# Optimization experiments

Hardware: AMD Instinct MI355X
Metric: run time of the kernel (lower is better)

The kernel has to match this reference:

```python
import jax, jax.numpy as jnp
import numpy as np

# physical constants / config (from __init__ defaults + chosen kwargs)
WFA_C = 4.6686e-13   # e/(4*pi*m_e*c) in 1/(G*Angstrom)
LAMBDA0 = 6301.5     # Angstrom
G_FACTOR = 1.5
WFA_WEIGHT = 0.5
STOKES_V = 3
BLOS_THRESH = 100.0
BASE_THRESH = 0.0004
TAU_IDX = np.array([0, 1, 2])
N_LOGTAU, N_MAGS = 21, 4
NWL = 112
START, END = 0, NWL - 1  # wavelength_range=None -> [0, len-1) slice
EPS = 1e-10


def _np_gradient(x):
    """np.gradient along last axis: central diffs interior, one-sided edges."""
    left = x[..., 1:2] - x[..., 0:1]
    mid = (x[..., 2:] - x[..., :-2]) * 0.5
    right = x[..., -1:] - x[..., -2:-1]
    return jnp.concatenate([left, mid, right], axis=-1)


def setup_inputs() -> dict:
    key = jax.random.key(0)
    kS, kP, kT = jax.random.split(key, 3)
    B = 65536
    input_stokes = jax.random.normal(kS, (B, 4, NWL), dtype=jnp.float32) * 0.01
    predicted_atm = jax.random.normal(kP, (B, N_LOGTAU * N_MAGS), dtype=jnp.float32)
    # target close to prediction so base MAE < base_loss_threshold -> WFA branch active
    target_atm = predicted_atm + 1e-4 * jax.random.normal(kT, (B, N_LOGTAU * N_MAGS), dtype=jnp.float32)
    wavelengths = jnp.linspace(6300.5, 6303.0, NWL).astype(jnp.float32)
    return {"input_stokes": input_stokes, "predicted_atm": predicted_atm,
            "target_atm": target_atm, "wavelengths": wavelengths}


def reference(input_stokes, predicted_atm, target_atm, wavelengths):
    # base MAE loss
    base_loss = jnp.mean(jnp.abs(predicted_atm - target_atm))

    # --- WFA B_LOS estimate, vectorized over batch ---
    wl = wavelengths[START:END]                      # [L]
    I = input_stokes[:, 0, START:END]                # [B, L]
    V = input_stokes[:, STOKES_V, START:END]         # [B, L]
    dI = _np_gradient(I) / _np_gradient(wl)[None, :]  # dI/dlambda, [B, L]

    # least squares V ~ p0*dI + p1; 2-column pinv == closed-form normal equations
    n = jnp.float32(dI.shape[-1])
    sd = jnp.sum(dI, axis=-1)
    sv = jnp.sum(V, axis=-1)
    sdd = jnp.sum(dI * dI, axis=-1)
    sdv = jnp.sum(dI * V, axis=-1)
    p0 = (n * sdv - sd * sv) / (n * sdd - sd * sd)   # slope, [B]
    wfa_blos = -p0 / (WFA_C * LAMBDA0 ** 2 * G_FACTOR)  # Gauss, [B]

    # predicted B_LOS: mean over tau_indices of last magnetic parameter
    atm = predicted_atm.reshape(-1, N_LOGTAU, N_MAGS)
    predicted_blos = atm[:, TAU_IDX, -1].mean(axis=1)  # [B]

    # thresholded masked log-abs MAE
    mask = jnp.abs(wfa_blos) < BLOS_THRESH
    diff = jnp.abs(jnp.log10(jnp.abs(predicted_blos) + EPS)
                   - jnp.log10(jnp.abs(wfa_blos) + EPS))
    cnt = jnp.sum(mask)
    wfa_loss_masked = jnp.sum(jnp.where(mask, diff, 0.0)) / jnp.maximum(cnt, 1).astype(diff.dtype)

    # early-return semantics: WFA only if base_loss < threshold AND any mask
    apply_wfa = (base_loss < BASE_THRESH) & (cnt > 0)
    wfa_loss = jnp.where(apply_wfa, wfa_loss_masked, jnp.float32(0.0))
    total_loss = jnp.where(apply_wfa,
                           (1.0 - WFA_WEIGHT) * base_loss + WFA_WEIGHT * wfa_loss_masked,
                           base_loss)
    return total_loss, base_loss, wfa_loss
```

## Files before the change

### kernel.cpp

```cpp
#include <hip/hip_runtime.h>
#include <math.h>

#define NWL   112
#define NCOLS 111
#define NATM  84
#define THREADS 256
#define WAVES_PER_BLOCK 4
#define MAIN_BLOCKS 2048

__device__ __forceinline__ float half_reduce_sum(float v) {
    v += __shfl_xor(v, 1,  64);
    v += __shfl_xor(v, 2,  64);
    v += __shfl_xor(v, 4,  64);
    v += __shfl_xor(v, 8,  64);
    v += __shfl_xor(v, 16, 64);
    return v;
}

__device__ __forceinline__ float wave_reduce_sum(float v) {
#pragma unroll
    for (int off = 32; off >= 1; off >>= 1)
        v += __shfl_xor(v, off, 64);
    return v;
}

__global__ __launch_bounds__(THREADS) void wfa_main(
    const float* __restrict__ stokes,
    const float* __restrict__ pred,
    const float* __restrict__ targ,
    const float* __restrict__ wl,
    float* __restrict__ ws,
    int nrows, int nblocks)
{
    __shared__ float s_idw[NWL];
    __shared__ float s_red[WAVES_PER_BLOCK][3];

    const int tid  = threadIdx.x;
    const int lane = tid & 63;
    const int wid  = tid >> 6;
    const int sub  = lane & 31;
    const int g    = lane & 32;

    if (tid < NWL) {
        const int j = tid;
        float d;
        if (j == 0)              d = wl[1] - wl[0];
        else if (j == NCOLS - 1) d = wl[NCOLS - 1] - wl[NCOLS - 2];
        else if (j < NCOLS - 1)  d = 0.5f * (wl[j + 1] - wl[j - 1]);
        else                     d = 1.0f;
        s_idw[j] = (j == NCOLS) ? 0.0f : 1.0f / d;
    }
    __syncthreads();

    float4 idw4 = make_float4(0.f, 0.f, 0.f, 0.f);
    if (sub < 28) idw4 = *(const float4*)&s_idw[4 * sub];

    const float WFA_DEN = (float)(4.6686e-13 * 6301.5 * 6301.5 * 1.5);

    const int h  = (blockIdx.x * WAVES_PER_BLOCK + wid) * 2 + (lane >> 5);
    const int nh = nblocks * WAVES_PER_BLOCK * 2;

    float base_acc = 0.f;
    float wfa_acc  = 0.f;
    float cnt_acc  = 0.f;

    for (int r = h; r < nrows; r += nh) {
        const float* rowbase = stokes + (size_t)r * (4 * NWL);

        float4 I4 = make_float4(0.f, 0.f, 0.f, 0.f);
        float4 V4 = make_float4(0.f, 0.f, 0.f, 0.f);
        if (sub < 28) {
            I4 = ((const float4*)rowbase)[sub];
            V4 = ((const float4*)(rowbase + 3 * NWL))[sub];
        }

        float4 P4 = make_float4(0.f, 0.f, 0.f, 0.f);
        float bpart = 0.f;
        if (sub < 21) {
            P4 = ((const float4*)(pred + (size_t)r * NATM))[sub];
            const float4 T4 = ((const float4*)(targ + (size_t)r * NATM))[sub];
            bpart = fabsf(P4.x - T4.x) + fabsf(P4.y - T4.y)
                  + fabsf(P4.z - T4.z) + fabsf(P4.w - T4.w);
        }
        base_acc += bpart;

        const int lm1 = lane - (sub ? 1 : 0);
        const float im1 = __shfl(I4.w, lm1, 64);
        const float ip4 = __shfl(I4.x, lane + 1, 64);

        const float n0 = (sub == 0)  ? (I4.y - I4.x) : 0.5f * (I4.y - im1);
        const float n1 = 0.5f * (I4.z - I4.x);
        const float n2 = (sub == 27) ? (I4.z - I4.y) : 0.5f * (I4.w - I4.y);
        const float n3 = 0.5f * (ip4 - I4.z);

        const float d0 = n0 * idw4.x;
        const float d1 = n1 * idw4.y;
        const float d2 = n2 * idw4.z;
        const float d3 = n3 * idw4.w;
        const float v3 = (sub == 27) ? 0.f : V4.w;

        float sd  = d0 + d1 + d2 + d3;
        float sdd = fmaf(d0, d0, fmaf(d1, d1, fmaf(d2, d2, d3 * d3)));
        float sdv = fmaf(d0, V4.x, fmaf(d1, V4.y, fmaf(d2, V4.z, d3 * v3)));
        float sv  = V4.x + V4.y + V4.z + v3;

        sd  = half_reduce_sum(sd);
        sdd = half_reduce_sum(sdd);
        sdv = half_reduce_sum(sdv);
        sv  = half_reduce_sum(sv);

        const float a7  = __shfl(P4.w, g | 1, 64);
        const float a11 = __shfl(P4.w, g | 2, 64);

        if (sub == 0) {
            const float n  = (float)NCOLS;
            const float p0 = (n * sdv - sd * sv) / (n * sdd - sd * sd);
            const float ab = fabsf(p0) / WFA_DEN;
            if (ab < 100.0f) {
                const float pb = (P4.w + a7 + a11) / 3.0f;
                wfa_acc += fabsf(log10f(fabsf(pb) + 1e-10f) - log10f(ab + 1e-10f));
                cnt_acc += 1.0f;
            }
        }
    }

    base_acc = wave_reduce_sum(base_acc);
    wfa_acc  = wave_reduce_sum(wfa_acc);
    cnt_acc  = wave_reduce_sum(cnt_acc);
    if (lane == 0) {
        s_red[wid][0] = base_acc;
        s_red[wid][1] = wfa_acc;
        s_red[wid][2] = cnt_acc;
    }
    __syncthreads();
    if (tid == 0) {
        float b = 0.f, w = 0.f, c = 0.f;
#pragma unroll
        for (int k = 0; k < WAVES_PER_BLOCK; ++k) {
            b += s_red[k][0]; w += s_red[k][1]; c += s_red[k][2];
        }
        ws[blockIdx.x]               = b;
        ws[nblocks + blockIdx.x]     = w;
        ws[2 * nblocks + blockIdx.x] = c;
    }
}

__global__ __launch_bounds__(256) void wfa_final(
    const float* __restrict__ ws, float* __restrict__ out,
    int nblocks, int nrows)
{
    const int tid = threadIdx.x;
    float b = 0.f, w = 0.f, c = 0.f;
    for (int i = tid; i < nblocks; i += 256) {
        b += ws[i];
        w += ws[nblocks + i];
        c += ws[2 * nblocks + i];
    }
    b = wave_reduce_sum(b);
    w = wave_reduce_sum(w);
    c = wave_reduce_sum(c);

    __shared__ float sb[4], sw[4], sc[4];
    const int lane = tid & 63, wid = tid >> 6;
    if (lane == 0) { sb[wid] = b; sw[wid] = w; sc[wid] = c; }
    __syncthreads();
    if (tid == 0) {
        const float B_ = sb[0] + sb[1] + sb[2] + sb[3];
        const float W_ = sw[0] + sw[1] + sw[2] + sw[3];
        const float C_ = sc[0] + sc[1] + sc[2] + sc[3];
        const float base_loss = B_ / (float)((long long)nrows * NATM);
        const float wfa_ml    = W_ / fmaxf(C_, 1.0f);
        const bool  apply     = (base_loss < 0.0004f) && (C_ > 0.f);
        out[0] = apply ? (0.5f * base_loss + 0.5f * wfa_ml) : base_loss;
        out[1] = base_loss;
        out[2] = apply ? wfa_ml : 0.f;
    }
}

extern "C" void kernel_launch(void* const* d_in, const int* in_sizes, int n_in,
                              void* d_out, int out_size, void* d_ws, size_t ws_size,
                              hipStream_t stream)
{
    const float* stokes = (const float*)d_in[0];
    const float* pred   = (const float*)d_in[1];
    const float* targ   = (const float*)d_in[2];
    const float* wl     = (const float*)d_in[3];
    float* out = (float*)d_out;
    float* ws  = (float*)d_ws;

    const int nrows = in_sizes[1] / NATM;

    int nblocks = MAIN_BLOCKS;
    const size_t need = (size_t)nblocks * 3 * sizeof(float);
    if (ws_size < need) {
        nblocks = (int)(ws_size / (3 * sizeof(float)));
        if (nblocks < 1) nblocks = 1;
    }

    hipLaunchKernelGGL(wfa_main, dim3(nblocks), dim3(THREADS), 0, stream,
                       stokes, pred, targ, wl, ws, nrows, nblocks);
    hipLaunchKernelGGL(wfa_final, dim3(1), dim3(256), 0, stream,
                       ws, out, nblocks, nrows);
}
```

Before: 196.8 us.

## Use DPP/swizzle half-wave reductions and nontemporal loads for streaming inputs

Replaces the shfl_xor-based 32-lane reductions with DPP row operations and ds_swizzle, so fewer LDS-permute instructions sit on the per-row critical path. All streaming loads of Stokes, prediction and target rows become nontemporal, which is meant to reduce cache pollution. The shuffles for the tau-index values are hoisted ahead of the reductions so they can overlap. The main risk is the correctness of the DPP and swizzle patterns: they must reproduce the xor 1/2/4/8/16 butterfly exactly within each 32-lane half.

Result: faster. 186.6 us (-5.2%).

```diff
diff --git a/kernel.cpp b/kernel.cpp
--- a/kernel.cpp
+++ b/kernel.cpp
@@ -8,12 +8,25 @@
 #define WAVES_PER_BLOCK 4
 #define MAIN_BLOCKS 2048
 
+typedef float f4v __attribute__((ext_vector_type(4)));
+
+template<int CTRL>
+__device__ __forceinline__ float dpp_add(float v) {
+    int x = __builtin_amdgcn_update_dpp(0, __float_as_int(v), CTRL, 0xF, 0xF, true);
+    return v + __int_as_float(x);
+}
+template<int PAT>
+__device__ __forceinline__ float swz_add(float v) {
+    int x = __builtin_amdgcn_ds_swizzle(__float_as_int(v), PAT);
+    return v + __int_as_float(x);
+}
+
 __device__ __forceinline__ float half_reduce_sum(float v) {
-    v += __shfl_xor(v, 1,  64);
-    v += __shfl_xor(v, 2,  64);
-    v += __shfl_xor(v, 4,  64);
-    v += __shfl_xor(v, 8,  64);
-    v += __shfl_xor(v, 16, 64);
+    v = dpp_add<0xB1>(v);
+    v = dpp_add<0x4E>(v);
+    v = swz_add<0x101F>(v);
+    v = dpp_add<0x128>(v);
+    v = swz_add<0x401F>(v);
     return v;
 }
 
@@ -70,23 +83,28 @@
         float4 I4 = make_float4(0.f, 0.f, 0.f, 0.f);
         float4 V4 = make_float4(0.f, 0.f, 0.f, 0.f);
         if (sub < 28) {
-            I4 = ((const float4*)rowbase)[sub];
-            V4 = ((const float4*)(rowbase + 3 * NWL))[sub];
+            f4v iv = __builtin_nontemporal_load((const f4v*)rowbase + sub);
+            f4v vv = __builtin_nontemporal_load((const f4v*)(rowbase + 3 * NWL) + sub);
+            I4 = make_float4(iv.x, iv.y, iv.z, iv.w);
+            V4 = make_float4(vv.x, vv.y, vv.z, vv.w);
         }
 
         float4 P4 = make_float4(0.f, 0.f, 0.f, 0.f);
         float bpart = 0.f;
         if (sub < 21) {
-            P4 = ((const float4*)(pred + (size_t)r * NATM))[sub];
-            const float4 T4 = ((const float4*)(targ + (size_t)r * NATM))[sub];
-            bpart = fabsf(P4.x - T4.x) + fabsf(P4.y - T4.y)
-                  + fabsf(P4.z - T4.z) + fabsf(P4.w - T4.w);
+            f4v pv = __builtin_nontemporal_load((const f4v*)(pred + (size_t)r * NATM) + sub);
+            f4v tv = __builtin_nontemporal_load((const f4v*)(targ + (size_t)r * NATM) + sub);
+            P4 = make_float4(pv.x, pv.y, pv.z, pv.w);
+            bpart = fabsf(pv.x - tv.x) + fabsf(pv.y - tv.y)
+                  + fabsf(pv.z - tv.z) + fabsf(pv.w - tv.w);
         }
         base_acc += bpart;
 
         const int lm1 = lane - (sub ? 1 : 0);
         const float im1 = __shfl(I4.w, lm1, 64);
         const float ip4 = __shfl(I4.x, lane + 1, 64);
+        const float a7  = __shfl(P4.w, g | 1, 64);
+        const float a11 = __shfl(P4.w, g | 2, 64);
 
         const float n0 = (sub == 0)  ? (I4.y - I4.x) : 0.5f * (I4.y - im1);
         const float n1 = 0.5f * (I4.z - I4.x);
@@ -108,9 +126,6 @@
         sdd = half_reduce_sum(sdd);
         sdv = half_reduce_sum(sdv);
         sv  = half_reduce_sum(sv);
-
-        const float a7  = __shfl(P4.w, g | 1, 64);
-        const float a11 = __shfl(P4.w, g | 2, 64);
 
         if (sub == 0) {
             const float n  = (float)NCOLS;
```
